# Kernel tuning notes

Measured on AMD Instinct MI355X. Metric: run time of the kernel, lower is better.

Reference implementation:

```python
import jax, jax.numpy as jnp
import numpy as np

M = 7          # window size
SHIFT = 3      # window_size // 2 (shift=True)
NUM_HEADS = 4


def _relative_position_index(m):
    coords = np.stack(np.meshgrid(np.arange(m), np.arange(m), indexing='ij')).reshape(2, -1)
    rel = (coords[:, :, None] - coords[:, None, :]).transpose(1, 2, 0).copy()  # (N,N,2)
    rel[..., 0] += m - 1
    rel[..., 1] += m - 1
    rel[..., 0] *= 2 * m - 1
    return rel.sum(-1).astype(np.int32)  # (N,N)


def _shift_attn_mask(H, W, m, s):
    img = np.zeros((H, W), np.float32)
    cnt = 0
    for hs in (slice(0, -m), slice(-m, -s), slice(-s, None)):
        for ws in (slice(0, -m), slice(-m, -s), slice(-s, None)):
            img[hs, ws] = cnt
            cnt += 1
    mw = img.reshape(H // m, m, W // m, m).transpose(0, 2, 1, 3).reshape(-1, m * m)  # (nW, N)
    diff = mw[:, None, :] - mw[:, :, None]
    return np.where(diff != 0, np.float32(-100.0), np.float32(0.0))  # (nW, N, N)


def setup_inputs():
    key = jax.random.key(0)
    k0, k1, k2, k3 = jax.random.split(key, 4)
    B, C, H, W = 32, 128, 112, 112
    h = NUM_HEADS
    x = jax.random.normal(k0, (B, C, H, W), jnp.float32)
    norm_w = jnp.ones((C,), jnp.float32)
    norm_b = jnp.zeros((C,), jnp.float32)
    qkv_w = jax.random.normal(k1, (3 * C, C), jnp.float32) * 0.02
    qkv_b = jnp.zeros((3 * C,), jnp.float32)
    proj_w = jax.random.normal(k2, (C, C), jnp.float32) * 0.02
    proj_b = jnp.zeros((C,), jnp.float32)
    bias_table = jax.random.normal(k3, ((2 * M - 1) ** 2, h), jnp.float32) * 0.02
    rel_index = jnp.asarray(_relative_position_index(M))
    attn_mask = jnp.asarray(_shift_attn_mask(H, W, M, SHIFT))
    return dict(x=x, norm_w=norm_w, norm_b=norm_b, qkv_w=qkv_w, qkv_b=qkv_b,
                proj_w=proj_w, proj_b=proj_b, bias_table=bias_table,
                rel_index=rel_index, attn_mask=attn_mask)


def reference(x, norm_w, norm_b, qkv_w, qkv_b, proj_w, proj_b, bias_table, rel_index, attn_mask):
    B, C, H, W = x.shape
    h = bias_table.shape[1]
    d = C // h
    N = M * M
    nH, nW = H // M, W // M

    xp = jnp.transpose(x, (0, 2, 3, 1))  # (B,H,W,C)
    shortcut = xp
    mu = xp.mean(-1, keepdims=True)
    var = ((xp - mu) ** 2).mean(-1, keepdims=True)
    xn = (xp - mu) / jnp.sqrt(var + 1e-5) * norm_w + norm_b

    xn = jnp.roll(xn, (-SHIFT, -SHIFT), (1, 2))  # cyclic shift

    # window partition -> (B*nH*nW, N, C)
    w = xn.reshape(B, nH, M, nW, M, C).transpose((0, 1, 3, 2, 4, 5)).reshape(-1, N, C)

    qkv = w @ qkv_w.T + qkv_b  # (B_, N, 3C)
    qkv = qkv.reshape(-1, N, 3, h, d).transpose((2, 0, 3, 1, 4))  # (3, B_, h, N, d)
    q, k, v = qkv[0], qkv[1], qkv[2]

    attn = jnp.einsum('bhnd,bhmd->bhnm', q, k) * (d ** -0.5)  # (B_, h, N, N)
    bias = bias_table[rel_index.reshape(-1)].reshape(N, N, h).transpose((2, 0, 1))  # (h,N,N)
    attn = attn + bias[None]

    nWnd = attn_mask.shape[0]  # number of windows per image
    attn = attn.reshape(B, nWnd, h, N, N) + attn_mask[None, :, None]
    attn = attn.reshape(-1, h, N, N)

    p = jax.nn.softmax(attn, axis=-1)
    o = jnp.einsum('bhnm,bhmd->bhnd', p, v).transpose((0, 2, 1, 3)).reshape(-1, N, C)
    o = o @ proj_w.T + proj_b

    # window reverse -> (B,H,W,C)
    o = o.reshape(B, nH, nW, M, M, C).transpose((0, 1, 3, 2, 4, 5)).reshape(B, H, W, C)
    o = jnp.roll(o, (SHIFT, SHIFT), (1, 2))  # reverse shift

    return jnp.transpose(shortcut + o, (0, 3, 1, 2))  # (B,C,H,W)
```

## Files before the change

kernel.cpp:

```cpp
#include <hip/hip_runtime.h>
#include <hip/hip_bf16.h>

typedef __attribute__((ext_vector_type(8))) short bf16x8;
typedef __attribute__((ext_vector_type(4))) float f32x4;
typedef __attribute__((ext_vector_type(8))) unsigned short ushort8;

__device__ __forceinline__ float bf2f(unsigned short u) {
  union { unsigned int i; float f; } v; v.i = ((unsigned int)u) << 16; return v.f;
}
__device__ __forceinline__ unsigned short f2bf(float f) {
  __hip_bfloat16 h = __float2bfloat16(f);
  unsigned short u; __builtin_memcpy(&u, &h, 2); return u;
}

__global__ void k_prep(const float* __restrict__ qkvw, const float* __restrict__ projw,
                       unsigned short* __restrict__ qkvw_bf,
                       unsigned short* __restrict__ projw_bf) {
  int t = blockIdx.x * 256 + threadIdx.x;
  int i = t * 4;
  const float* src;
  unsigned short* dst;
  int idx;
  if (i < 49152) { src = qkvw; dst = qkvw_bf; idx = i; }
  else           { src = projw; dst = projw_bf; idx = i - 49152; }
  float4 v = *(const float4*)(src + idx);
  union { unsigned short u[4]; uint2 v2; } o;
  o.u[0] = f2bf(v.x); o.u[1] = f2bf(v.y); o.u[2] = f2bf(v.z); o.u[3] = f2bf(v.w);
  *(uint2*)(dst + idx) = o.v2;
}

__global__ void k_bias(const float* __restrict__ bt,
                       const int* __restrict__ ri,
                       float* __restrict__ b2d) {
  int t = blockIdx.x * 256 + threadIdx.x;
  if (t < 9604) {
    int hq = t / 2401;
    int rc = t - hq * 2401;
    b2d[t] = bt[ri[rc] * 4 + hq];
  }
}

__global__ __launch_bounds__(256, 4) void k_ln(const float* __restrict__ x,
                                               const float* __restrict__ nw,
                                               const float* __restrict__ nb,
                                               unsigned short* __restrict__ xw) {
  int p = blockIdx.x * 256 + threadIdx.x;
  int b = p / 12544;
  int r = p - b * 12544;
  int hh = r / 112;
  int wp = r - hh * 112;
  const float* bx = x + (size_t)b * 1605632 + r;

  float sum = 0.f, ss = 0.f;
  #pragma unroll 16
  for (int c = 0; c < 128; ++c) {
    float v = bx[(size_t)c * 12544];
    sum += v; ss += v * v;
  }
  float mu = sum * 0.0078125f;
  float var = ss * 0.0078125f - mu * mu;
  float rstd = rsqrtf(var + 1e-5f);

  int h2 = hh + 109; if (h2 >= 112) h2 -= 112;
  int w2 = wp + 109; if (w2 >= 112) w2 -= 112;
  int wh = h2 / 7, ii = h2 - wh * 7;
  int ww = w2 / 7, jj = w2 - ww * 7;
  int winl = (b * 16 + wh) * 16 + ww;
  unsigned short* dst = xw + ((size_t)winl * 49 + ii * 7 + jj) * 128;

  #pragma unroll
  for (int g = 0; g < 4; ++g) {
    unsigned int pk[16];
    #pragma unroll
    for (int q = 0; q < 16; ++q) {
      int c = g * 32 + 2 * q;
      float v0 = bx[(size_t)c * 12544];
      float v1 = bx[(size_t)(c + 1) * 12544];
      float y0 = (v0 - mu) * rstd * nw[c]     + nb[c];
      float y1 = (v1 - mu) * rstd * nw[c + 1] + nb[c + 1];
      pk[q] = (unsigned int)f2bf(y0) | ((unsigned int)f2bf(y1) << 16);
    }
    uint4* d4 = (uint4*)(dst + g * 32);
    #pragma unroll
    for (int k = 0; k < 4; ++k)
      d4[k] = make_uint4(pk[4 * k], pk[4 * k + 1], pk[4 * k + 2], pk[4 * k + 3]);
  }
}

__global__ __launch_bounds__(256, 2) void k_attn(
    const unsigned short* __restrict__ xw,
    const unsigned short* __restrict__ qkvw,
    const float* __restrict__ qkvb,
    const unsigned short* __restrict__ projw,
    const float* __restrict__ projb,
    const float* __restrict__ b2d,
    const float* __restrict__ amask,
    unsigned short* __restrict__ yw) {
  __shared__ __attribute__((aligned(16))) char smem[59392];
  const int tid  = threadIdx.x;
  const int lane = tid & 63;
  const int h    = tid >> 6;
  const int m15  = lane & 15;
  const int quad = lane >> 4;
  const int win  = blockIdx.x;
  const int b    = win >> 8;
  const int wrem = win & 255;
  const int wh   = wrem >> 4;
  const int ww   = wrem & 15;
  const f32x4 fz = {0.f, 0.f, 0.f, 0.f};

  {
    const uint4* gsrc = (const uint4*)(xw + (size_t)win * 6272);
    #pragma unroll
    for (int it = 0; it < 4; ++it) {
      int cc = tid + it * 256;
      int row = cc >> 4, col = cc & 15;
      uint4 v = make_uint4(0u, 0u, 0u, 0u);
      if (cc < 784) v = gsrc[cc];
      *(uint4*)(smem + row * 272 + col * 16) = v;
    }
  }
  __syncthreads();

  bf16x8 xf[4][4];
  #pragma unroll
  for (int mt = 0; mt < 4; ++mt)
    #pragma unroll
    for (int kt = 0; kt < 4; ++kt)
      xf[mt][kt] = *(const bf16x8*)(smem + (mt * 16 + m15) * 272 + kt * 64 + quad * 16);
  __syncthreads();

  char* const hb  = smem + h * 14848;
  char* const qpb = hb;
  char* const kpb = hb + 5120;
  char* const vpb = hb + 10240;

  #pragma unroll
  for (int g = 0; g < 3; ++g) {
    #pragma unroll
    for (int sp = 0; sp < 2; ++sp) {
      int nt = g * 8 + 2 * h + sp;
      int f = nt * 16 + m15;
      bf16x8 wfr[4];
      #pragma unroll
      for (int kt = 0; kt < 4; ++kt)
        wfr[kt] = *(const bf16x8*)(qkvw + f * 128 + kt * 32 + quad * 8);
      float bias = qkvb[f];
      int dsub = sp * 16 + m15;
      #pragma unroll
      for (int mt = 0; mt < 4; ++mt) {
        f32x4 acc = fz;
        #pragma unroll
        for (int kt = 0; kt < 4; ++kt)
          acc = __builtin_amdgcn_mfma_f32_16x16x32_bf16(xf[mt][kt], wfr[kt], acc, 0, 0, 0);
        #pragma unroll
        for (int rr = 0; rr < 4; ++rr) {
          int token = mt * 16 + quad * 4 + rr;
          unsigned short val = f2bf(acc[rr] + bias);
          if (g == 0)      *(unsigned short*)(qpb + token * 80 + dsub * 2) = val;
          else if (g == 1) *(unsigned short*)(kpb + token * 80 + dsub * 2) = val;
          else             *(unsigned short*)(vpb + dsub * 144 + token * 2) = val;
        }
      }
    }
  }

  bf16x8 qf[4], kf[4];
  #pragma unroll
  for (int t = 0; t < 4; ++t) {
    qf[t] = *(const bf16x8*)(qpb + (t * 16 + m15) * 80 + quad * 16);
    kf[t] = *(const bf16x8*)(kpb + (t * 16 + m15) * 80 + quad * 16);
  }
  f32x4 sacc[4][4];
  #pragma unroll
  for (int mt = 0; mt < 4; ++mt)
    #pragma unroll
    for (int nt = 0; nt < 4; ++nt)
      sacc[mt][nt] = __builtin_amdgcn_mfma_f32_16x16x32_bf16(qf[mt], kf[nt], fz, 0, 0, 0);

  const float* bp = b2d + h * 2401;
  const float* mp = amask + wrem * 2401;
  #pragma unroll
  for (int mt = 0; mt < 4; ++mt) {
    #pragma unroll
    for (int rr = 0; rr < 4; ++rr) {
      int row = mt * 16 + quad * 4 + rr;
      int rb = row * 49;
      float sv[4];
      #pragma unroll
      for (int nt = 0; nt < 4; ++nt) {
        int col = nt * 16 + m15;
        float s = -1e30f;
        if (row < 49 && col < 49)
          s = sacc[mt][nt][rr] * 0.17677669529663687f + bp[rb + col] + mp[rb + col];
        sv[nt] = s;
      }
      float mx = fmaxf(fmaxf(sv[0], sv[1]), fmaxf(sv[2], sv[3]));
      mx = fmaxf(mx, __shfl_xor(mx, 1));
      mx = fmaxf(mx, __shfl_xor(mx, 2));
      mx = fmaxf(mx, __shfl_xor(mx, 4));
      mx = fmaxf(mx, __shfl_xor(mx, 8));
      float pv[4]; float sum = 0.f;
      #pragma unroll
      for (int nt = 0; nt < 4; ++nt) { pv[nt] = __expf(sv[nt] - mx); sum += pv[nt]; }
      sum += __shfl_xor(sum, 1);
      sum += __shfl_xor(sum, 2);
      sum += __shfl_xor(sum, 4);
      sum += __shfl_xor(sum, 8);
      float rinv = 1.0f / sum;
      #pragma unroll
      for (int nt = 0; nt < 4; ++nt)
        *(unsigned short*)(qpb + row * 144 + (nt * 16 + m15) * 2) = f2bf(pv[nt] * rinv);
    }
  }

  f32x4 oacc[4][2];
  #pragma unroll
  for (int mt = 0; mt < 4; ++mt) {
    #pragma unroll
    for (int nt = 0; nt < 2; ++nt) {
      f32x4 acc = fz;
      #pragma unroll
      for (int kt = 0; kt < 2; ++kt) {
        bf16x8 pf = *(const bf16x8*)(qpb + (mt * 16 + m15) * 144 + kt * 64 + quad * 16);
        bf16x8 vf = *(const bf16x8*)(vpb + (nt * 16 + m15) * 144 + kt * 64 + quad * 16);
        acc = __builtin_amdgcn_mfma_f32_16x16x32_bf16(pf, vf, acc, 0, 0, 0);
      }
      oacc[mt][nt] = acc;
    }
  }
  #pragma unroll
  for (int mt = 0; mt < 4; ++mt)
    #pragma unroll
    for (int nt = 0; nt < 2; ++nt)
      #pragma unroll
      for (int rr = 0; rr < 4; ++rr) {
        int token = mt * 16 + quad * 4 + rr;
        *(unsigned short*)(qpb + token * 80 + (nt * 16 + m15) * 2) = f2bf(oacc[mt][nt][rr]);
      }
  __syncthreads();

  bf16x8 of[4][4];
  #pragma unroll
  for (int mt = 0; mt < 4; ++mt)
    #pragma unroll
    for (int kt = 0; kt < 4; ++kt)
      of[mt][kt] = *(const bf16x8*)(smem + kt * 14848 + (mt * 16 + m15) * 80 + quad * 16);

  const size_t obase = (size_t)b * 1605632;
  #pragma unroll
  for (int sp = 0; sp < 2; ++sp) {
    int cout = (2 * h + sp) * 16 + m15;
    bf16x8 wf[4];
    #pragma unroll
    for (int kt = 0; kt < 4; ++kt)
      wf[kt] = *(const bf16x8*)(projw + cout * 128 + kt * 32 + quad * 8);
    float pb = projb[cout];
    #pragma unroll
    for (int mt = 0; mt < 4; ++mt) {
      f32x4 acc = fz;
      #pragma unroll
      for (int kt = 0; kt < 4; ++kt)
        acc = __builtin_amdgcn_mfma_f32_16x16x32_bf16(of[mt][kt], wf[kt], acc, 0, 0, 0);
      #pragma unroll
      for (int rr = 0; rr < 4; ++rr) {
        int token = mt * 16 + quad * 4 + rr;
        if (token < 49) {
          int ii = token / 7, jj = token - ii * 7;
          int gh = wh * 7 + ii + 3; if (gh >= 112) gh -= 112;
          int gw = ww * 7 + jj + 3; if (gw >= 112) gw -= 112;
          yw[obase + ((size_t)(gh * 112 + gw)) * 128 + cout] = f2bf(acc[rr] + pb);
        }
      }
    }
  }
}

__global__ __launch_bounds__(256) void k_out(const unsigned short* __restrict__ yws,
                                             const float* __restrict__ x,
                                             float* __restrict__ out) {
  __shared__ unsigned short T[128 * 128];
  int tid = threadIdx.x;
  int bid = blockIdx.x;
  int b = bid / 112;
  int hh = bid - b * 112;
  const unsigned short* src = yws + (size_t)(b * 112 + hh) * 14336;
  #pragma unroll
  for (int it = 0; it < 7; ++it) {
    int cc = tid + it * 256;
    int w = cc >> 4, c8 = (cc & 15) * 8;
    ushort8 v = *(const ushort8*)(src + w * 128 + c8);
    #pragma unroll
    for (int k = 0; k < 8; ++k) T[(c8 + k) * 128 + w] = v[k];
  }
  __syncthreads();
  int c = tid >> 1, half = tid & 1;
  size_t rowoff = ((size_t)(b * 128 + c) * 112 + hh) * 112;
  const float* xr = x + rowoff;
  float* outr = out + rowoff;
  #pragma unroll
  for (int s2 = 0; s2 < 7; ++s2) {
    int w = half * 56 + s2 * 8;
    ushort8 yv = *(const ushort8*)(T + c * 128 + w);
    float4 xa = *(const float4*)(xr + w);
    float4 xb = *(const float4*)(xr + w + 4);
    float4 oa, ob;
    oa.x = bf2f(yv[0]) + xa.x; oa.y = bf2f(yv[1]) + xa.y;
    oa.z = bf2f(yv[2]) + xa.z; oa.w = bf2f(yv[3]) + xa.w;
    ob.x = bf2f(yv[4]) + xb.x; ob.y = bf2f(yv[5]) + xb.y;
    ob.z = bf2f(yv[6]) + xb.z; ob.w = bf2f(yv[7]) + xb.w;
    *(float4*)(outr + w) = oa;
    *(float4*)(outr + w + 4) = ob;
  }
}

extern "C" void kernel_launch(void* const* d_in, const int* in_sizes, int n_in,
                              void* d_out, int out_size, void* d_ws, size_t ws_size,
                              hipStream_t stream) {
  const float* x     = (const float*)d_in[0];
  const float* nw    = (const float*)d_in[1];
  const float* nb    = (const float*)d_in[2];
  const float* qkvw  = (const float*)d_in[3];
  const float* qkvb  = (const float*)d_in[4];
  const float* projw = (const float*)d_in[5];
  const float* projb = (const float*)d_in[6];
  const float* bt    = (const float*)d_in[7];
  const int*   ri    = (const int*)d_in[8];
  const float* am    = (const float*)d_in[9];

  unsigned short* xw   = (unsigned short*)d_ws;
  unsigned short* yws  = (unsigned short*)((char*)d_ws + 102760448);
  float*          b2d  = (float*)((char*)d_ws + 205520896);
  unsigned short* qwbf = (unsigned short*)((char*)d_ws + 205559312);
  unsigned short* pwbf = (unsigned short*)((char*)d_ws + 205657616);
  float* out = (float*)d_out;

  k_prep<<<64,   256, 0, stream>>>(qkvw, projw, qwbf, pwbf);
  k_bias<<<38,   256, 0, stream>>>(bt, ri, b2d);
  k_ln  <<<1568, 256, 0, stream>>>(x, nw, nb, xw);
  k_attn<<<8192, 256, 0, stream>>>(xw, qwbf, qkvb, pwbf, projb, b2d, am, yws);
  k_out <<<3584, 256, 0, stream>>>(yws, x, out);
}
```

Measured before the change: 818.8 us.

## Restructure window attention to 512 threads with transposed MFMA and padded bias/mask

Rewrites the attention kernel to use 8 waves per window, splitting tokens into halves per head. QK^T and PV are computed in transposed form so each lane writes packed vectors. Softmax skips the max subtraction and combines partial row sums through shared memory. Bias and mask are pre-padded to 64 columns, with the mask stored as bf16, so the kernel can use vector loads. LayerNorm now caches x as bf16 in registers instead of reading it twice, which adds rounding error, and the output transpose moves to a padded row-major LDS layout. Dropping the max subtraction relies on the scores staying small enough not to overflow exp.

Result: slower. 866.5 us (+5.8%).

```diff
diff --git a/kernel.cpp b/kernel.cpp
--- a/kernel.cpp
+++ b/kernel.cpp
@@ -5,12 +5,15 @@
 typedef __attribute__((ext_vector_type(4))) float f32x4;
 typedef __attribute__((ext_vector_type(8))) unsigned short ushort8;
 
-__device__ __forceinline__ float bf2f(unsigned short u) {
-  union { unsigned int i; float f; } v; v.i = ((unsigned int)u) << 16; return v.f;
+__device__ __forceinline__ float bf2f(unsigned int u) {
+  union { unsigned int i; float f; } v; v.i = u << 16; return v.f;
 }
 __device__ __forceinline__ unsigned short f2bf(float f) {
   __hip_bfloat16 h = __float2bfloat16(f);
   unsigned short u; __builtin_memcpy(&u, &h, 2); return u;
+}
+__device__ __forceinline__ unsigned int pk2(float a, float b) {
+  return (unsigned int)f2bf(a) | ((unsigned int)f2bf(b) << 16);
 }
 
 __global__ void k_prep(const float* __restrict__ qkvw, const float* __restrict__ projw,
@@ -24,20 +27,25 @@
   if (i < 49152) { src = qkvw; dst = qkvw_bf; idx = i; }
   else           { src = projw; dst = projw_bf; idx = i - 49152; }
   float4 v = *(const float4*)(src + idx);
-  union { unsigned short u[4]; uint2 v2; } o;
-  o.u[0] = f2bf(v.x); o.u[1] = f2bf(v.y); o.u[2] = f2bf(v.z); o.u[3] = f2bf(v.w);
-  *(uint2*)(dst + idx) = o.v2;
-}
-
-__global__ void k_bias(const float* __restrict__ bt,
-                       const int* __restrict__ ri,
-                       float* __restrict__ b2d) {
+  uint2 o; o.x = pk2(v.x, v.y); o.y = pk2(v.z, v.w);
+  *(uint2*)(dst + idx) = o;
+}
+
+__global__ void k_biasp(const float* __restrict__ bt, const int* __restrict__ ri,
+                        float* __restrict__ b2dp) {
   int t = blockIdx.x * 256 + threadIdx.x;
-  if (t < 9604) {
-    int hq = t / 2401;
-    int rc = t - hq * 2401;
-    b2d[t] = bt[ri[rc] * 4 + hq];
-  }
+  int h = t / 3136;
+  int r = t - h * 3136;
+  int q = r >> 6, k = r & 63;
+  b2dp[t] = (k < 49) ? bt[ri[q * 49 + k] * 4 + h] : 0.f;
+}
+
+__global__ void k_maskp(const float* __restrict__ am, unsigned short* __restrict__ maskp) {
+  int t = blockIdx.x * 256 + threadIdx.x;
+  int w = t / 3136;
+  int r = t - w * 3136;
+  int q = r >> 6, k = r & 63;
+  maskp[t] = f2bf((k < 49) ? am[w * 2401 + q * 49 + k] : -100.f);
 }
 
 __global__ __launch_bounds__(256, 4) void k_ln(const float* __restrict__ x,
@@ -51,11 +59,14 @@
   int wp = r - hh * 112;
   const float* bx = x + (size_t)b * 1605632 + r;
 
+  unsigned int xb[64];
   float sum = 0.f, ss = 0.f;
-  #pragma unroll 16
-  for (int c = 0; c < 128; ++c) {
-    float v = bx[(size_t)c * 12544];
-    sum += v; ss += v * v;
+  #pragma unroll
+  for (int cg = 0; cg < 64; ++cg) {
+    float v0 = bx[(size_t)(2 * cg) * 12544];
+    float v1 = bx[(size_t)(2 * cg + 1) * 12544];
+    sum += v0 + v1; ss += v0 * v0 + v1 * v1;
+    xb[cg] = pk2(v0, v1);
   }
   float mu = sum * 0.0078125f;
   float var = ss * 0.0078125f - mu * mu;
@@ -70,36 +81,40 @@
 
   #pragma unroll
   for (int g = 0; g < 4; ++g) {
-    unsigned int pk[16];
+    unsigned int pkk[16];
     #pragma unroll
     for (int q = 0; q < 16; ++q) {
-      int c = g * 32 + 2 * q;
-      float v0 = bx[(size_t)c * 12544];
-      float v1 = bx[(size_t)(c + 1) * 12544];
-      float y0 = (v0 - mu) * rstd * nw[c]     + nb[c];
+      int cg = g * 16 + q;
+      unsigned int u = xb[cg];
+      float v0 = bf2f(u & 0xffffu), v1 = bf2f(u >> 16);
+      int c = 2 * cg;
+      float y0 = (v0 - mu) * rstd * nw[c] + nb[c];
       float y1 = (v1 - mu) * rstd * nw[c + 1] + nb[c + 1];
-      pk[q] = (unsigned int)f2bf(y0) | ((unsigned int)f2bf(y1) << 16);
+      pkk[q] = pk2(y0, y1);
     }
     uint4* d4 = (uint4*)(dst + g * 32);
     #pragma unroll
     for (int k = 0; k < 4; ++k)
-      d4[k] = make_uint4(pk[4 * k], pk[4 * k + 1], pk[4 * k + 2], pk[4 * k + 3]);
-  }
-}
-
-__global__ __launch_bounds__(256, 2) void k_attn(
+      d4[k] = make_uint4(pkk[4 * k], pkk[4 * k + 1], pkk[4 * k + 2], pkk[4 * k + 3]);
+  }
+}
+
+__global__ __launch_bounds__(512, 4) void k_attn(
     const unsigned short* __restrict__ xw,
     const unsigned short* __restrict__ qkvw,
     const float* __restrict__ qkvb,
     const unsigned short* __restrict__ projw,
     const float* __restrict__ projb,
-    const float* __restrict__ b2d,
-    const float* __restrict__ amask,
+    const float* __restrict__ b2dp,
+    const unsigned short* __restrict__ maskp,
     unsigned short* __restrict__ yw) {
-  __shared__ __attribute__((aligned(16))) char smem[59392];
+  __shared__ __attribute__((aligned(16))) char smem[61440];
+  float* part = (float*)(smem + 59392);
   const int tid  = threadIdx.x;
   const int lane = tid & 63;
-  const int h    = tid >> 6;
+  const int wid  = tid >> 6;
+  const int h    = wid & 3;
+  const int half = wid >> 2;
   const int m15  = lane & 15;
   const int quad = lane >> 4;
   const int win  = blockIdx.x;
@@ -112,8 +127,8 @@
   {
     const uint4* gsrc = (const uint4*)(xw + (size_t)win * 6272);
     #pragma unroll
-    for (int it = 0; it < 4; ++it) {
-      int cc = tid + it * 256;
+    for (int it = 0; it < 2; ++it) {
+      int cc = tid + it * 512;
       int row = cc >> 4, col = cc & 15;
       uint4 v = make_uint4(0u, 0u, 0u, 0u);
       if (cc < 784) v = gsrc[cc];
@@ -121,157 +136,174 @@
     }
   }
   __syncthreads();
-
-  bf16x8 xf[4][4];
-  #pragma unroll
-  for (int mt = 0; mt < 4; ++mt)
+  bf16x8 xf[2][4];
+  #pragma unroll
+  for (int t = 0; t < 2; ++t)
     #pragma unroll
     for (int kt = 0; kt < 4; ++kt)
-      xf[mt][kt] = *(const bf16x8*)(smem + (mt * 16 + m15) * 272 + kt * 64 + quad * 16);
-  __syncthreads();
-
-  char* const hb  = smem + h * 14848;
-  char* const qpb = hb;
-  char* const kpb = hb + 5120;
-  char* const vpb = hb + 10240;
-
-  #pragma unroll
-  for (int g = 0; g < 3; ++g) {
-    #pragma unroll
-    for (int sp = 0; sp < 2; ++sp) {
-      int nt = g * 8 + 2 * h + sp;
-      int f = nt * 16 + m15;
-      bf16x8 wfr[4];
+      xf[t][kt] = *(const bf16x8*)(smem + ((half * 2 + t) * 16 + m15) * 272 + kt * 64 + quad * 16);
+  __syncthreads();
+
+  char* const Hq = smem + h * 14848;
+  char* const Hk = Hq + 5120;
+  char* const Hv = Hq + 10240;
+
+  #pragma unroll
+  for (int g = 0; g < 2; ++g) {
+    char* dst = g ? Hk : Hq;
+    #pragma unroll
+    for (int ft = 0; ft < 2; ++ft) {
+      int grow = g * 128 + h * 32 + ft * 16 + m15;
+      bf16x8 wf[4];
       #pragma unroll
       for (int kt = 0; kt < 4; ++kt)
-        wfr[kt] = *(const bf16x8*)(qkvw + f * 128 + kt * 32 + quad * 8);
-      float bias = qkvb[f];
-      int dsub = sp * 16 + m15;
+        wf[kt] = *(const bf16x8*)(qkvw + grow * 128 + kt * 32 + quad * 8);
+      float4 b4 = *(const float4*)(qkvb + g * 128 + h * 32 + ft * 16 + 4 * quad);
       #pragma unroll
-      for (int mt = 0; mt < 4; ++mt) {
+      for (int t = 0; t < 2; ++t) {
         f32x4 acc = fz;
         #pragma unroll
         for (int kt = 0; kt < 4; ++kt)
-          acc = __builtin_amdgcn_mfma_f32_16x16x32_bf16(xf[mt][kt], wfr[kt], acc, 0, 0, 0);
-        #pragma unroll
-        for (int rr = 0; rr < 4; ++rr) {
-          int token = mt * 16 + quad * 4 + rr;
-          unsigned short val = f2bf(acc[rr] + bias);
-          if (g == 0)      *(unsigned short*)(qpb + token * 80 + dsub * 2) = val;
-          else if (g == 1) *(unsigned short*)(kpb + token * 80 + dsub * 2) = val;
-          else             *(unsigned short*)(vpb + dsub * 144 + token * 2) = val;
-        }
+          acc = __builtin_amdgcn_mfma_f32_16x16x32_bf16(wf[kt], xf[t][kt], acc, 0, 0, 0);
+        int token = (half * 2 + t) * 16 + m15;
+        uint2 u;
+        u.x = pk2(acc[0] + b4.x, acc[1] + b4.y);
+        u.y = pk2(acc[2] + b4.z, acc[3] + b4.w);
+        *(uint2*)(dst + token * 80 + ft * 32 + 8 * quad) = u;
       }
     }
   }
-
-  bf16x8 qf[4], kf[4];
-  #pragma unroll
-  for (int t = 0; t < 4; ++t) {
-    qf[t] = *(const bf16x8*)(qpb + (t * 16 + m15) * 80 + quad * 16);
-    kf[t] = *(const bf16x8*)(kpb + (t * 16 + m15) * 80 + quad * 16);
-  }
-  f32x4 sacc[4][4];
-  #pragma unroll
-  for (int mt = 0; mt < 4; ++mt)
-    #pragma unroll
-    for (int nt = 0; nt < 4; ++nt)
-      sacc[mt][nt] = __builtin_amdgcn_mfma_f32_16x16x32_bf16(qf[mt], kf[nt], fz, 0, 0, 0);
-
-  const float* bp = b2d + h * 2401;
-  const float* mp = amask + wrem * 2401;
-  #pragma unroll
-  for (int mt = 0; mt < 4; ++mt) {
-    #pragma unroll
-    for (int rr = 0; rr < 4; ++rr) {
-      int row = mt * 16 + quad * 4 + rr;
-      int rb = row * 49;
-      float sv[4];
-      #pragma unroll
-      for (int nt = 0; nt < 4; ++nt) {
-        int col = nt * 16 + m15;
-        float s = -1e30f;
-        if (row < 49 && col < 49)
-          s = sacc[mt][nt][rr] * 0.17677669529663687f + bp[rb + col] + mp[rb + col];
-        sv[nt] = s;
-      }
-      float mx = fmaxf(fmaxf(sv[0], sv[1]), fmaxf(sv[2], sv[3]));
-      mx = fmaxf(mx, __shfl_xor(mx, 1));
-      mx = fmaxf(mx, __shfl_xor(mx, 2));
-      mx = fmaxf(mx, __shfl_xor(mx, 4));
-      mx = fmaxf(mx, __shfl_xor(mx, 8));
-      float pv[4]; float sum = 0.f;
-      #pragma unroll
-      for (int nt = 0; nt < 4; ++nt) { pv[nt] = __expf(sv[nt] - mx); sum += pv[nt]; }
-      sum += __shfl_xor(sum, 1);
-      sum += __shfl_xor(sum, 2);
-      sum += __shfl_xor(sum, 4);
-      sum += __shfl_xor(sum, 8);
-      float rinv = 1.0f / sum;
-      #pragma unroll
-      for (int nt = 0; nt < 4; ++nt)
-        *(unsigned short*)(qpb + row * 144 + (nt * 16 + m15) * 2) = f2bf(pv[nt] * rinv);
-    }
-  }
-
-  f32x4 oacc[4][2];
-  #pragma unroll
-  for (int mt = 0; mt < 4; ++mt) {
-    #pragma unroll
-    for (int nt = 0; nt < 2; ++nt) {
-      f32x4 acc = fz;
-      #pragma unroll
-      for (int kt = 0; kt < 2; ++kt) {
-        bf16x8 pf = *(const bf16x8*)(qpb + (mt * 16 + m15) * 144 + kt * 64 + quad * 16);
-        bf16x8 vf = *(const bf16x8*)(vpb + (nt * 16 + m15) * 144 + kt * 64 + quad * 16);
-        acc = __builtin_amdgcn_mfma_f32_16x16x32_bf16(pf, vf, acc, 0, 0, 0);
-      }
-      oacc[mt][nt] = acc;
-    }
-  }
-  #pragma unroll
-  for (int mt = 0; mt < 4; ++mt)
-    #pragma unroll
-    for (int nt = 0; nt < 2; ++nt)
-      #pragma unroll
-      for (int rr = 0; rr < 4; ++rr) {
-        int token = mt * 16 + quad * 4 + rr;
-        *(unsigned short*)(qpb + token * 80 + (nt * 16 + m15) * 2) = f2bf(oacc[mt][nt][rr]);
-      }
-  __syncthreads();
-
-  bf16x8 of[4][4];
-  #pragma unroll
-  for (int mt = 0; mt < 4; ++mt)
+  #pragma unroll
+  for (int ntd = 0; ntd < 2; ++ntd) {
+    int vrow = 256 + h * 32 + ntd * 16 + m15;
+    bf16x8 wv[4];
     #pragma unroll
     for (int kt = 0; kt < 4; ++kt)
-      of[mt][kt] = *(const bf16x8*)(smem + kt * 14848 + (mt * 16 + m15) * 80 + quad * 16);
-
-  const size_t obase = (size_t)b * 1605632;
-  #pragma unroll
-  for (int sp = 0; sp < 2; ++sp) {
-    int cout = (2 * h + sp) * 16 + m15;
-    bf16x8 wf[4];
-    #pragma unroll
-    for (int kt = 0; kt < 4; ++kt)
-      wf[kt] = *(const bf16x8*)(projw + cout * 128 + kt * 32 + quad * 8);
-    float pb = projb[cout];
-    #pragma unroll
-    for (int mt = 0; mt < 4; ++mt) {
+      wv[kt] = *(const bf16x8*)(qkvw + vrow * 128 + kt * 32 + quad * 8);
+    float vb = qkvb[vrow];
+    #pragma unroll
+    for (int t = 0; t < 2; ++t) {
       f32x4 acc = fz;
       #pragma unroll
       for (int kt = 0; kt < 4; ++kt)
-        acc = __builtin_amdgcn_mfma_f32_16x16x32_bf16(of[mt][kt], wf[kt], acc, 0, 0, 0);
+        acc = __builtin_amdgcn_mfma_f32_16x16x32_bf16(xf[t][kt], wv[kt], acc, 0, 0, 0);
+      int dim = ntd * 16 + m15;
+      uint2 u;
+      u.x = pk2(acc[0] + vb, acc[1] + vb);
+      u.y = pk2(acc[2] + vb, acc[3] + vb);
+      *(uint2*)(Hv + dim * 144 + ((half * 2 + t) * 16 + 4 * quad) * 2) = u;
+    }
+  }
+  __syncthreads();
+
+  bf16x8 ka[2], qb[4];
+  #pragma unroll
+  for (int mk = 0; mk < 2; ++mk)
+    ka[mk] = *(const bf16x8*)(Hk + ((half * 2 + mk) * 16 + m15) * 80 + quad * 16);
+  #pragma unroll
+  for (int nt = 0; nt < 4; ++nt)
+    qb[nt] = *(const bf16x8*)(Hq + (nt * 16 + m15) * 80 + quad * 16);
+  f32x4 sacc[2][4];
+  #pragma unroll
+  for (int mk = 0; mk < 2; ++mk)
+    #pragma unroll
+    for (int nt = 0; nt < 4; ++nt)
+      sacc[mk][nt] = __builtin_amdgcn_mfma_f32_16x16x32_bf16(ka[mk], qb[nt], fz, 0, 0, 0);
+
+  #pragma unroll
+  for (int nt = 0; nt < 4; ++nt) {
+    int query = nt * 16 + m15;
+    float ls = 0.f;
+    #pragma unroll
+    for (int mk = 0; mk < 2; ++mk) {
+      int kb = (half * 2 + mk) * 16 + 4 * quad;
+      float bm0 = 0.f, bm1 = 0.f, bm2 = 0.f, bm3 = 0.f;
+      if (query < 49) {
+        float4 bb = *(const float4*)(b2dp + (h * 49 + query) * 64 + kb);
+        uint2 mm = *(const uint2*)(maskp + (wrem * 49 + query) * 64 + kb);
+        bm0 = bb.x + bf2f(mm.x & 0xffffu);
+        bm1 = bb.y + bf2f(mm.x >> 16);
+        bm2 = bb.z + bf2f(mm.y & 0xffffu);
+        bm3 = bb.w + bf2f(mm.y >> 16);
+      }
+      float s0 = (query < 49) ? fmaf(sacc[mk][nt][0], 0.17677669529663687f, bm0) : 0.f;
+      float s1 = (query < 49) ? fmaf(sacc[mk][nt][1], 0.17677669529663687f, bm1) : 0.f;
+      float s2 = (query < 49) ? fmaf(sacc[mk][nt][2], 0.17677669529663687f, bm2) : 0.f;
+      float s3 = (query < 49) ? fmaf(sacc[mk][nt][3], 0.17677669529663687f, bm3) : 0.f;
+      float e0 = __expf(s0), e1 = __expf(s1), e2 = __expf(s2), e3 = __expf(s3);
+      sacc[mk][nt][0] = e0; sacc[mk][nt][1] = e1;
+      sacc[mk][nt][2] = e2; sacc[mk][nt][3] = e3;
+      ls += e0 + e1 + e2 + e3;
+    }
+    ls += __shfl_xor(ls, 16);
+    ls += __shfl_xor(ls, 32);
+    if (quad == 0) part[h * 128 + query * 2 + half] = ls;
+  }
+  __syncthreads();
+  #pragma unroll
+  for (int nt = 0; nt < 4; ++nt) {
+    int query = nt * 16 + m15;
+    float2 pq = *(const float2*)(part + h * 128 + query * 2);
+    float rinv = 1.f / (pq.x + pq.y);
+    #pragma unroll
+    for (int mk = 0; mk < 2; ++mk) {
+      uint2 u;
+      u.x = pk2(sacc[mk][nt][0] * rinv, sacc[mk][nt][1] * rinv);
+      u.y = pk2(sacc[mk][nt][2] * rinv, sacc[mk][nt][3] * rinv);
+      *(uint2*)(Hq + query * 144 + ((half * 2 + mk) * 16 + 4 * quad) * 2) = u;
+    }
+  }
+  __syncthreads();
+
+  bf16x8 va[2][2], pfr[2][2];
+  #pragma unroll
+  for (int mtd = 0; mtd < 2; ++mtd)
+    #pragma unroll
+    for (int kt = 0; kt < 2; ++kt)
+      va[mtd][kt] = *(const bf16x8*)(Hv + (mtd * 16 + m15) * 144 + kt * 64 + quad * 16);
+  #pragma unroll
+  for (int t = 0; t < 2; ++t)
+    #pragma unroll
+    for (int kt = 0; kt < 2; ++kt)
+      pfr[t][kt] = *(const bf16x8*)(Hq + ((half * 2 + t) * 16 + m15) * 144 + kt * 64 + quad * 16);
+  #pragma unroll
+  for (int mtd = 0; mtd < 2; ++mtd)
+    #pragma unroll
+    for (int t = 0; t < 2; ++t) {
+      f32x4 acc = fz;
       #pragma unroll
-      for (int rr = 0; rr < 4; ++rr) {
-        int token = mt * 16 + quad * 4 + rr;
-        if (token < 49) {
-          int ii = token / 7, jj = token - ii * 7;
-          int gh = wh * 7 + ii + 3; if (gh >= 112) gh -= 112;
-          int gw = ww * 7 + jj + 3; if (gw >= 112) gw -= 112;
-          yw[obase + ((size_t)(gh * 112 + gw)) * 128 + cout] = f2bf(acc[rr] + pb);
-        }
-      }
+      for (int kt = 0; kt < 2; ++kt)
+        acc = __builtin_amdgcn_mfma_f32_16x16x32_bf16(va[mtd][kt], pfr[t][kt], acc, 0, 0, 0);
+      int query = (half * 2 + t) * 16 + m15;
+      uint2 u; u.x = pk2(acc[0], acc[1]); u.y = pk2(acc[2], acc[3]);
+      *(uint2*)(Hq + query * 144 + (mtd * 16 + 4 * quad) * 2) = u;
+    }
+  __syncthreads();
+
+  const int mtc = wid;
+  bf16x8 awf[4];
+  #pragma unroll
+  for (int kt = 0; kt < 4; ++kt)
+    awf[kt] = *(const bf16x8*)(projw + (mtc * 16 + m15) * 128 + kt * 32 + quad * 8);
+  float4 pb4 = *(const float4*)(projb + mtc * 16 + 4 * quad);
+  const size_t obase = (size_t)b * 1605632;
+  #pragma unroll
+  for (int nt = 0; nt < 4; ++nt) {
+    f32x4 acc = fz;
+    #pragma unroll
+    for (int kt = 0; kt < 4; ++kt) {
+      bf16x8 ob = *(const bf16x8*)(smem + kt * 14848 + (nt * 16 + m15) * 144 + quad * 16);
+      acc = __builtin_amdgcn_mfma_f32_16x16x32_bf16(awf[kt], ob, acc, 0, 0, 0);
+    }
+    int token = nt * 16 + m15;
+    if (token < 49) {
+      int ii = token / 7, jj = token - ii * 7;
+      int gh = wh * 7 + ii + 3; if (gh >= 112) gh -= 112;
+      int gw = ww * 7 + jj + 3; if (gw >= 112) gw -= 112;
+      uint2 u;
+      u.x = pk2(acc[0] + pb4.x, acc[1] + pb4.y);
+      u.y = pk2(acc[2] + pb4.z, acc[3] + pb4.w);
+      *(uint2*)(yw + obase + (size_t)(gh * 112 + gw) * 128 + mtc * 16 + 4 * quad) = u;
     }
   }
 }
@@ -279,7 +311,7 @@
 __global__ __launch_bounds__(256) void k_out(const unsigned short* __restrict__ yws,
                                              const float* __restrict__ x,
                                              float* __restrict__ out) {
-  __shared__ unsigned short T[128 * 128];
+  __shared__ unsigned short T[112 * 136];
   int tid = threadIdx.x;
   int bid = blockIdx.x;
   int b = bid / 112;
@@ -290,8 +322,7 @@
     int cc = tid + it * 256;
     int w = cc >> 4, c8 = (cc & 15) * 8;
     ushort8 v = *(const ushort8*)(src + w * 128 + c8);
-    #pragma unroll
-    for (int k = 0; k < 8; ++k) T[(c8 + k) * 128 + w] = v[k];
+    *(ushort8*)(T + w * 136 + c8) = v;
   }
   __syncthreads();
   int c = tid >> 1, half = tid & 1;
@@ -301,14 +332,17 @@
   #pragma unroll
   for (int s2 = 0; s2 < 7; ++s2) {
     int w = half * 56 + s2 * 8;
-    ushort8 yv = *(const ushort8*)(T + c * 128 + w);
     float4 xa = *(const float4*)(xr + w);
     float4 xb = *(const float4*)(xr + w + 4);
     float4 oa, ob;
-    oa.x = bf2f(yv[0]) + xa.x; oa.y = bf2f(yv[1]) + xa.y;
-    oa.z = bf2f(yv[2]) + xa.z; oa.w = bf2f(yv[3]) + xa.w;
-    ob.x = bf2f(yv[4]) + xb.x; ob.y = bf2f(yv[5]) + xb.y;
-    ob.z = bf2f(yv[6]) + xb.z; ob.w = bf2f(yv[7]) + xb.w;
+    oa.x = bf2f(T[(w + 0) * 136 + c]) + xa.x;
+    oa.y = bf2f(T[(w + 1) * 136 + c]) + xa.y;
+    oa.z = bf2f(T[(w + 2) * 136 + c]) + xa.z;
+    oa.w = bf2f(T[(w + 3) * 136 + c]) + xa.w;
+    ob.x = bf2f(T[(w + 4) * 136 + c]) + xb.x;
+    ob.y = bf2f(T[(w + 5) * 136 + c]) + xb.y;
+    ob.z = bf2f(T[(w + 6) * 136 + c]) + xb.z;
+    ob.w = bf2f(T[(w + 7) * 136 + c]) + xb.w;
     *(float4*)(outr + w) = oa;
     *(float4*)(outr + w + 4) = ob;
   }
@@ -328,16 +362,18 @@
   const int*   ri    = (const int*)d_in[8];
   const float* am    = (const float*)d_in[9];
 
-  unsigned short* xw   = (unsigned short*)d_ws;
-  unsigned short* yws  = (unsigned short*)((char*)d_ws + 102760448);
-  float*          b2d  = (float*)((char*)d_ws + 205520896);
-  unsigned short* qwbf = (unsigned short*)((char*)d_ws + 205559312);
-  unsigned short* pwbf = (unsigned short*)((char*)d_ws + 205657616);
+  unsigned short* xw    = (unsigned short*)d_ws;
+  unsigned short* yws   = (unsigned short*)((char*)d_ws + 102760448);
+  float*          b2dp  = (float*)((char*)d_ws + 205520896);
+  unsigned short* maskp = (unsigned short*)((char*)d_ws + 205571072);
+  unsigned short* qwbf  = (unsigned short*)((char*)d_ws + 207176704);
+  unsigned short* pwbf  = (unsigned short*)((char*)d_ws + 207275008);
   float* out = (float*)d_out;
 
-  k_prep<<<64,   256, 0, stream>>>(qkvw, projw, qwbf, pwbf);
-  k_bias<<<38,   256, 0, stream>>>(bt, ri, b2d);
-  k_ln  <<<1568, 256, 0, stream>>>(x, nw, nb, xw);
-  k_attn<<<8192, 256, 0, stream>>>(xw, qwbf, qkvb, pwbf, projb, b2d, am, yws);
-  k_out <<<3584, 256, 0, stream>>>(yws, x, out);
-}
+  k_prep <<<64,   256, 0, stream>>>(qkvw, projw, qwbf, pwbf);
+  k_biasp<<<49,   256, 0, stream>>>(bt, ri, b2dp);
+  k_maskp<<<3136, 256, 0, stream>>>(am, maskp);
+  k_ln   <<<1568, 256, 0, stream>>>(x, nw, nb, xw);
+  k_attn <<<8192, 512, 0, stream>>>(xw, qwbf, qkvb, pwbf, projb, b2dp, maskp, yws);
+  k_out  <<<3584, 256, 0, stream>>>(yws, x, out);
+}
```
